# Kernel tuning notes

Hardware: AMD Instinct MI355X
Metric: run time of the kernel (lower is better)

The kernel has to match this reference:

```python
import jax, jax.numpy as jnp
import numpy as np

B, S, D, H = 2, 2048, 1024, 16
HD = D // H  # head_dim = 64


def setup_inputs() -> dict:
    key = jax.random.key(0)
    k1, k2, k3 = jax.random.split(key, 3)
    x = jax.random.normal(k1, (B, S, D), dtype=jnp.float32)
    mask = jnp.zeros((B, S, S), dtype=jnp.float32)  # additive mask
    # Dense(3*D) params (glorot-ish scale) and Dense(D) output projection
    Wqkv = jax.random.normal(k2, (D, 3 * D), dtype=jnp.float32) * (1.0 / np.sqrt(D))
    bqkv = jnp.zeros((3 * D,), dtype=jnp.float32)
    Wo = jax.random.normal(k3, (D, D), dtype=jnp.float32) * (1.0 / np.sqrt(D))
    bo = jnp.zeros((D,), dtype=jnp.float32)
    return {"x": x, "mask": mask, "Wqkv": Wqkv, "bqkv": bqkv, "Wo": Wo, "bo": bo}


def reference(x, mask, Wqkv, bqkv, Wo, bo):
    b, s, d = x.shape
    qkv = x @ Wqkv + bqkv                              # [B,S,3D]
    qkv = qkv.reshape(b, s, H, 3 * HD).transpose(0, 2, 1, 3)  # [B,H,S,3*HD]
    q, k, v = jnp.split(qkv, 3, axis=-1)               # each [B,H,S,HD]
    scale = 1.0 / jnp.sqrt(jnp.float32(HD))
    scores = jnp.einsum('bhqd,bhkd->bhqk', q, k) * scale  # [B,H,S,S]
    scores = scores + mask[:, None, :, :]
    attn = jax.nn.softmax(scores, axis=-1)
    values = jnp.einsum('bhqk,bhkd->bhqd', attn, v)    # [B,H,S,HD]
    # Faithful to original: reshape WITHOUT transposing heads back
    values = values.reshape(b, s, H * HD)              # [B,S,D]
    return values @ Wo + bo
```

## Files before the change

kernel.cpp:

```cpp
#include <hip/hip_runtime.h>
#include <hip/hip_bf16.h>

#define B_ 2
#define S_ 2048
#define D_ 1024
#define H_ 16
#define HD_ 64

typedef __attribute__((ext_vector_type(8))) short short8;
typedef __attribute__((ext_vector_type(4))) float f32x4;
typedef __attribute__((ext_vector_type(16))) float f32x16;
typedef __attribute__((ext_vector_type(4))) unsigned short us4;

static __device__ __forceinline__ ushort f2bf(float x) {
  __hip_bfloat16 h = __float2bfloat16(x);
  return *reinterpret_cast<ushort*>(&h);
}

static __device__ __forceinline__ void gld_lds16(void* lds, const void* g) {
  __builtin_amdgcn_global_load_lds(
      (__attribute__((address_space(1))) void*)(g),
      (__attribute__((address_space(3))) void*)(lds), 16, 0, 0);
}


__global__ __launch_bounds__(256) void cvt_bf16_vec(const float4* __restrict__ in,
                                                    ushort* __restrict__ out, int n4) {
  int i = blockIdx.x * blockDim.x + threadIdx.x;
  if (i < n4) {
    float4 v = in[i];
    ushort4 o;
    o.x = f2bf(v.x); o.y = f2bf(v.y); o.z = f2bf(v.z); o.w = f2bf(v.w);
    *reinterpret_cast<ushort4*>(out + (size_t)i * 4) = o;
  }
}

__global__ __launch_bounds__(256) void transpose_cvt(const float* __restrict__ in,
                                                     ushort* __restrict__ out,
                                                     int K, int N) {
  __shared__ float tile[32][33];
  const int bn = blockIdx.x * 32, bk = blockIdx.y * 32;
  const int tx = threadIdx.x, ty = threadIdx.y;
  #pragma unroll
  for (int i = ty; i < 32; i += 8)
    tile[i][tx] = in[(size_t)(bk + i) * N + bn + tx];
  __syncthreads();
  #pragma unroll
  for (int i = ty; i < 32; i += 8)
    out[(size_t)(bn + i) * K + bk + tx] = f2bf(tile[tx][i]);
}

template <bool OUT_BF16>
__global__ __launch_bounds__(256) void gemm_bt(const ushort* __restrict__ A,
                                               const ushort* __restrict__ Bt,
                                               const float* __restrict__ bias,
                                               ushort* __restrict__ Cb,
                                               float* __restrict__ Cf,
                                               int M, int N, int K) {
  __shared__ __align__(16) ushort As[128 * 32];
  __shared__ __align__(16) ushort Bs[128 * 32];
  const int tid = threadIdx.x;
  const int lane = tid & 63, wid = tid >> 6;
  const int wr = wid >> 1, wc = wid & 1;
  const int row0 = blockIdx.x * 128, col0 = blockIdx.y * 128;
  const int l15 = lane & 15, lhi = lane >> 4;

  f32x4 acc[4][4];
  #pragma unroll
  for (int i = 0; i < 4; ++i)
    #pragma unroll
    for (int j = 0; j < 4; ++j)
      acc[i][j] = f32x4{0.f, 0.f, 0.f, 0.f};

  const int sr = tid >> 2;
  const int scol = (tid & 3) * 8;

  for (int k0 = 0; k0 < K; k0 += 32) {
    gld_lds16(&As[(size_t)tid * 8],        &A[(size_t)(row0 + sr) * K + k0 + scol]);
    gld_lds16(&As[2048 + (size_t)tid * 8], &A[(size_t)(row0 + 64 + sr) * K + k0 + scol]);
    gld_lds16(&Bs[(size_t)tid * 8],        &Bt[(size_t)(col0 + sr) * K + k0 + scol]);
    gld_lds16(&Bs[2048 + (size_t)tid * 8], &Bt[(size_t)(col0 + 64 + sr) * K + k0 + scol]);
    __syncthreads();

    short8 af[4], bfr[4];
    #pragma unroll
    for (int mt = 0; mt < 4; ++mt)
      af[mt] = *(const short8*)&As[(wr * 64 + mt * 16 + l15) * 32 + lhi * 8];
    #pragma unroll
    for (int nt = 0; nt < 4; ++nt)
      bfr[nt] = *(const short8*)&Bs[(wc * 64 + nt * 16 + l15) * 32 + lhi * 8];
    #pragma unroll
    for (int mt = 0; mt < 4; ++mt)
      #pragma unroll
      for (int nt = 0; nt < 4; ++nt)
        acc[mt][nt] = __builtin_amdgcn_mfma_f32_16x16x32_bf16(af[mt], bfr[nt], acc[mt][nt], 0, 0, 0);
    __syncthreads();
  }

  const int orow = row0 + wr * 64;
  const int ocol = col0 + wc * 64 + l15;
  #pragma unroll
  for (int mt = 0; mt < 4; ++mt) {
    #pragma unroll
    for (int nt = 0; nt < 4; ++nt) {
      const int gc = ocol + nt * 16;
      const float bv = bias[gc];
      #pragma unroll
      for (int r = 0; r < 4; ++r) {
        const int gr = orow + mt * 16 + lhi * 4 + r;
        const float v = acc[mt][nt][r] + bv;
        if (OUT_BF16) Cb[(size_t)gr * N + gc] = f2bf(v);
        else          Cf[(size_t)gr * N + gc] = v;
      }
    }
  }
}

__global__ __launch_bounds__(256, 2) void flash_attn(const ushort* __restrict__ qkv,
                                                     const float* __restrict__ mask,
                                                     ushort* __restrict__ values) {
  __shared__ __align__(16) ushort Ks[2][64 * 64];
  __shared__ __align__(16) ushort Vt[2][64 * 64];

  const int tid = threadIdx.x;
  const int lane = tid & 63, wid = tid >> 6;
  const int l31 = lane & 31, lhalf = lane >> 5;
  const int qt = blockIdx.x, bh = blockIdx.y, b = bh >> 4, h = bh & 15;
  const size_t base = (size_t)b * S_ * 3072 + (size_t)h * 192;
  const int q = qt * 128 + wid * 32 + l31;

  short8 qf[4];
  {
    const ushort* qrow = qkv + base + (size_t)q * 3072 + lhalf * 8;
    qf[0] = *(const short8*)(qrow);
    qf[1] = *(const short8*)(qrow + 16);
    qf[2] = *(const short8*)(qrow + 32);
    qf[3] = *(const short8*)(qrow + 48);
  }

  const int srow = tid >> 3, sch = tid & 7;
  const int hsr = (srow ^ (srow >> 3)) & 7;
  const int scs = sch ^ hsr;
  const int kg = tid & 15, d0 = (tid >> 4) * 4;
  const int skg = (kg & 12) | ((kg & 1) << 1) | ((kg >> 1) & 1);

  float m_run = -3.0e38f, l_run = 0.f;
  f32x16 o[2];
  #pragma unroll
  for (int dg = 0; dg < 2; ++dg)
    #pragma unroll
    for (int i = 0; i < 16; ++i) o[dg][i] = 0.f;

  const float* mrow = mask + ((size_t)b * S_ + q) * S_;
  f32x4 mk[8], mkn[8];
  const int NT = S_ / 64;
  int cur = 0;
  us4 vr[4];

  {
    const ushort* kgp = qkv + base + (size_t)srow * 3072 + 64;
    gld_lds16(&Ks[0][tid * 8],        kgp + scs * 8);
    gld_lds16(&Ks[0][2048 + tid * 8], kgp + (size_t)32 * 3072 + (scs ^ 4) * 8);
    #pragma unroll
    for (int kk = 0; kk < 4; ++kk)
      vr[kk] = *(const us4*)(qkv + base + (size_t)(kg * 4 + kk) * 3072 + 128 + d0);
    #pragma unroll
    for (int i = 0; i < 8; ++i)
      mk[i] = *(const f32x4*)(mrow + (i >> 2) * 32 + (i & 3) * 8 + lhalf * 4);
    #pragma unroll
    for (int dd = 0; dd < 4; ++dd) {
      const int d = d0 + dd;
      const int hd = (d ^ (d >> 3)) & 7;
      us4 w;
      w[0] = vr[0][dd]; w[1] = vr[1][dd]; w[2] = vr[2][dd]; w[3] = vr[3][dd];
      *(us4*)&Vt[0][d * 64 + (((skg >> 1) ^ hd) & 7) * 8 + (skg & 1) * 4] = w;
    }
    __syncthreads();
  }

  for (int kt = 0; kt < NT; ++kt) {
    const int nxt = cur ^ 1;
    const bool pre = (kt + 1 < NT);

    if (pre) {
      const size_t nb = base + (size_t)(kt + 1) * 64 * 3072;
      const ushort* kgp = qkv + nb + (size_t)srow * 3072 + 64;
      gld_lds16(&Ks[nxt][tid * 8],        kgp + scs * 8);
      gld_lds16(&Ks[nxt][2048 + tid * 8], kgp + (size_t)32 * 3072 + (scs ^ 4) * 8);
      #pragma unroll
      for (int kk = 0; kk < 4; ++kk)
        vr[kk] = *(const us4*)(qkv + nb + (size_t)(kg * 4 + kk) * 3072 + 128 + d0);
      const float* mn = mrow + (size_t)(kt + 1) * 64;
      #pragma unroll
      for (int i = 0; i < 8; ++i)
        mkn[i] = *(const f32x4*)(mn + (i >> 2) * 32 + (i & 3) * 8 + lhalf * 4);
    }

    f32x16 sc[2];
    __builtin_amdgcn_s_setprio(1);
    #pragma unroll
    for (int g = 0; g < 2; ++g) {
      const int row = g * 32 + l31;
      const int hk = (row ^ (row >> 3)) & 7;
      const ushort* kp = &Ks[cur][row * 64];
      f32x16 s;
      #pragma unroll
      for (int i = 0; i < 16; ++i) s[i] = 0.f;
      #pragma unroll
      for (int kd = 0; kd < 4; ++kd) {
        short8 kf = *(const short8*)&kp[(((kd * 2 + lhalf) ^ hk) & 7) * 8];
        s = __builtin_amdgcn_mfma_f32_32x32x16_bf16(kf, qf[kd], s, 0, 0, 0);
      }
      sc[g] = s;
    }
    __builtin_amdgcn_s_setprio(0);

    #pragma unroll
    for (int g = 0; g < 2; ++g)
      #pragma unroll
      for (int r = 0; r < 16; ++r)
        sc[g][r] = sc[g][r] * 0.125f + mk[g * 4 + (r >> 2)][r & 3];

    float mx = sc[0][0];
    #pragma unroll
    for (int g = 0; g < 2; ++g)
      #pragma unroll
      for (int r = 0; r < 16; ++r) mx = fmaxf(mx, sc[g][r]);
    mx = fmaxf(mx, __shfl_xor(mx, 32));
    const float mnew = fmaxf(m_run, mx);
    const float alpha = __expf(m_run - mnew);
    m_run = mnew;
    float ps = 0.f;
    #pragma unroll
    for (int g = 0; g < 2; ++g)
      #pragma unroll
      for (int r = 0; r < 16; ++r) {
        const float p = __expf(sc[g][r] - mnew);
        sc[g][r] = p;
        ps += p;
      }
    ps += __shfl_xor(ps, 32);
    l_run = l_run * alpha + ps;
    #pragma unroll
    for (int dg = 0; dg < 2; ++dg)
      #pragma unroll
      for (int i = 0; i < 16; ++i) o[dg][i] *= alpha;

    short8 pf[4];
    #pragma unroll
    for (int ks = 0; ks < 4; ++ks)
      #pragma unroll
      for (int j = 0; j < 8; ++j)
        pf[ks][j] = (short)f2bf(sc[ks >> 1][8 * (ks & 1) + j]);

    __builtin_amdgcn_s_setprio(1);
    #pragma unroll
    for (int dg = 0; dg < 2; ++dg) {
      const int d = dg * 32 + l31;
      const int hv = (d ^ (d >> 3)) & 7;
      const ushort* vp = &Vt[cur][d * 64];
      #pragma unroll
      for (int ks = 0; ks < 4; ++ks) {
        short8 vf = *(const short8*)&vp[(((ks * 2 + lhalf) ^ hv) & 7) * 8];
        o[dg] = __builtin_amdgcn_mfma_f32_32x32x16_bf16(vf, pf[ks], o[dg], 0, 0, 0);
      }
    }
    __builtin_amdgcn_s_setprio(0);

    if (pre) {
      #pragma unroll
      for (int dd = 0; dd < 4; ++dd) {
        const int d = d0 + dd;
        const int hd = (d ^ (d >> 3)) & 7;
        us4 w;
        w[0] = vr[0][dd]; w[1] = vr[1][dd]; w[2] = vr[2][dd]; w[3] = vr[3][dd];
        *(us4*)&Vt[nxt][d * 64 + (((skg >> 1) ^ hd) & 7) * 8 + (skg & 1) * 4] = w;
      }
      #pragma unroll
      for (int i = 0; i < 8; ++i) mk[i] = mkn[i];
    }
    __syncthreads();
    cur = nxt;
  }

  const float inv = 1.0f / l_run;
  ushort* vout = values + ((size_t)bh * S_ + q) * 64;
  #pragma unroll
  for (int dg = 0; dg < 2; ++dg)
    #pragma unroll
    for (int quad = 0; quad < 4; ++quad) {
      us4 w;
      #pragma unroll
      for (int r = 0; r < 4; ++r) w[r] = f2bf(o[dg][quad * 4 + r] * inv);
      *(us4*)(vout + dg * 32 + quad * 8 + lhalf * 4) = w;
    }
}


extern "C" void kernel_launch(void* const* d_in, const int* in_sizes, int n_in,
                              void* d_out, int out_size, void* d_ws, size_t ws_size,
                              hipStream_t stream) {
  const float* x    = (const float*)d_in[0];
  const float* mask = (const float*)d_in[1];
  const float* Wqkv = (const float*)d_in[2];
  const float* bqkv = (const float*)d_in[3];
  const float* Wo   = (const float*)d_in[4];
  const float* bo   = (const float*)d_in[5];
  float* out = (float*)d_out;

  char* ws = (char*)d_ws;
  ushort* xbf    = (ushort*)(ws + 0);
  ushort* vals   = (ushort*)(ws + 0);
  ushort* wqkvT  = (ushort*)(ws + 8388608);
  ushort* woT    = (ushort*)(ws + 14680064);
  ushort* qkv    = (ushort*)(ws + 16777216);

  cvt_bf16_vec<<<4096, 256, 0, stream>>>((const float4*)x, xbf, (B_ * S_ * D_) / 4);
  transpose_cvt<<<dim3(3 * D_ / 32, D_ / 32), dim3(32, 8), 0, stream>>>(Wqkv, wqkvT, D_, 3 * D_);
  transpose_cvt<<<dim3(D_ / 32, D_ / 32), dim3(32, 8), 0, stream>>>(Wo, woT, D_, D_);
  gemm_bt<true><<<dim3((B_ * S_) / 128, (3 * D_) / 128), 256, 0, stream>>>(
      xbf, wqkvT, bqkv, qkv, nullptr, B_ * S_, 3 * D_, D_);
  flash_attn<<<dim3(S_ / 128, B_ * H_), 256, 0, stream>>>(qkv, mask, vals);
  gemm_bt<false><<<dim3((B_ * S_) / 128, D_ / 128), 256, 0, stream>>>(
      vals, woT, bo, nullptr, out, B_ * S_, D_, D_);
}
```

Measured before the change: 180.4 us.

## Process 128-key tiles per iteration with lazy softmax rescaling in flash attention

Doubles the key/value tile per loop iteration from 64 to 128 keys, with double-buffered LDS holding two 64-key subtiles per stage. This halves the number of barriers and softmax reductions per key. It also switches to a conditional online-softmax rescale that only updates the running max when it grows by more than 8, skipping the exponential and the accumulator multiply in most iterations. The mask is now loaded at the start of each iteration instead of being prefetched one tile ahead. This increases register pressure (16 mask vectors, 4 score tiles, 8 V staging registers) and LDS use to 64KB per block, which may lower occupancy under launch_bounds(256,2).

```diff
diff --git a/kernel.cpp b/kernel.cpp
--- a/kernel.cpp
+++ b/kernel.cpp
@@ -119,8 +119,8 @@
 __global__ __launch_bounds__(256, 2) void flash_attn(const ushort* __restrict__ qkv,
                                                      const float* __restrict__ mask,
                                                      ushort* __restrict__ values) {
-  __shared__ __align__(16) ushort Ks[2][64 * 64];
-  __shared__ __align__(16) ushort Vt[2][64 * 64];
+  __shared__ __align__(16) ushort Ks[2][2][64 * 64];
+  __shared__ __align__(16) ushort Vt[2][2][64 * 64];
 
   const int tid = threadIdx.x;
   const int lane = tid & 63, wid = tid >> 6;
@@ -152,132 +152,152 @@
     for (int i = 0; i < 16; ++i) o[dg][i] = 0.f;
 
   const float* mrow = mask + ((size_t)b * S_ + q) * S_;
-  f32x4 mk[8], mkn[8];
-  const int NT = S_ / 64;
+  const int NT2 = S_ / 128;
   int cur = 0;
-  us4 vr[4];
+  us4 vr[8];
 
   {
-    const ushort* kgp = qkv + base + (size_t)srow * 3072 + 64;
-    gld_lds16(&Ks[0][tid * 8],        kgp + scs * 8);
-    gld_lds16(&Ks[0][2048 + tid * 8], kgp + (size_t)32 * 3072 + (scs ^ 4) * 8);
-    #pragma unroll
-    for (int kk = 0; kk < 4; ++kk)
-      vr[kk] = *(const us4*)(qkv + base + (size_t)(kg * 4 + kk) * 3072 + 128 + d0);
-    #pragma unroll
-    for (int i = 0; i < 8; ++i)
-      mk[i] = *(const f32x4*)(mrow + (i >> 2) * 32 + (i & 3) * 8 + lhalf * 4);
-    #pragma unroll
-    for (int dd = 0; dd < 4; ++dd) {
-      const int d = d0 + dd;
-      const int hd = (d ^ (d >> 3)) & 7;
-      us4 w;
-      w[0] = vr[0][dd]; w[1] = vr[1][dd]; w[2] = vr[2][dd]; w[3] = vr[3][dd];
-      *(us4*)&Vt[0][d * 64 + (((skg >> 1) ^ hd) & 7) * 8 + (skg & 1) * 4] = w;
-    }
-    __syncthreads();
-  }
-
-  for (int kt = 0; kt < NT; ++kt) {
-    const int nxt = cur ^ 1;
-    const bool pre = (kt + 1 < NT);
-
-    if (pre) {
-      const size_t nb = base + (size_t)(kt + 1) * 64 * 3072;
-      const ushort* kgp = qkv + nb + (size_t)srow * 3072 + 64;
-      gld_lds16(&Ks[nxt][tid * 8],        kgp + scs * 8);
-      gld_lds16(&Ks[nxt][2048 + tid * 8], kgp + (size_t)32 * 3072 + (scs ^ 4) * 8);
+    #pragma unroll
+    for (int s2 = 0; s2 < 2; ++s2) {
+      const ushort* kgp = qkv + base + (size_t)(s2 * 64 + srow) * 3072 + 64;
+      gld_lds16(&Ks[0][s2][tid * 8],        kgp + scs * 8);
+      gld_lds16(&Ks[0][s2][2048 + tid * 8], kgp + (size_t)32 * 3072 + (scs ^ 4) * 8);
       #pragma unroll
       for (int kk = 0; kk < 4; ++kk)
-        vr[kk] = *(const us4*)(qkv + nb + (size_t)(kg * 4 + kk) * 3072 + 128 + d0);
-      const float* mn = mrow + (size_t)(kt + 1) * 64;
-      #pragma unroll
-      for (int i = 0; i < 8; ++i)
-        mkn[i] = *(const f32x4*)(mn + (i >> 2) * 32 + (i & 3) * 8 + lhalf * 4);
-    }
-
-    f32x16 sc[2];
-    __builtin_amdgcn_s_setprio(1);
-    #pragma unroll
-    for (int g = 0; g < 2; ++g) {
-      const int row = g * 32 + l31;
-      const int hk = (row ^ (row >> 3)) & 7;
-      const ushort* kp = &Ks[cur][row * 64];
-      f32x16 s;
-      #pragma unroll
-      for (int i = 0; i < 16; ++i) s[i] = 0.f;
-      #pragma unroll
-      for (int kd = 0; kd < 4; ++kd) {
-        short8 kf = *(const short8*)&kp[(((kd * 2 + lhalf) ^ hk) & 7) * 8];
-        s = __builtin_amdgcn_mfma_f32_32x32x16_bf16(kf, qf[kd], s, 0, 0, 0);
-      }
-      sc[g] = s;
-    }
-    __builtin_amdgcn_s_setprio(0);
-
-    #pragma unroll
-    for (int g = 0; g < 2; ++g)
-      #pragma unroll
-      for (int r = 0; r < 16; ++r)
-        sc[g][r] = sc[g][r] * 0.125f + mk[g * 4 + (r >> 2)][r & 3];
-
-    float mx = sc[0][0];
-    #pragma unroll
-    for (int g = 0; g < 2; ++g)
-      #pragma unroll
-      for (int r = 0; r < 16; ++r) mx = fmaxf(mx, sc[g][r]);
-    mx = fmaxf(mx, __shfl_xor(mx, 32));
-    const float mnew = fmaxf(m_run, mx);
-    const float alpha = __expf(m_run - mnew);
-    m_run = mnew;
-    float ps = 0.f;
-    #pragma unroll
-    for (int g = 0; g < 2; ++g)
-      #pragma unroll
-      for (int r = 0; r < 16; ++r) {
-        const float p = __expf(sc[g][r] - mnew);
-        sc[g][r] = p;
-        ps += p;
-      }
-    ps += __shfl_xor(ps, 32);
-    l_run = l_run * alpha + ps;
-    #pragma unroll
-    for (int dg = 0; dg < 2; ++dg)
-      #pragma unroll
-      for (int i = 0; i < 16; ++i) o[dg][i] *= alpha;
-
-    short8 pf[4];
-    #pragma unroll
-    for (int ks = 0; ks < 4; ++ks)
-      #pragma unroll
-      for (int j = 0; j < 8; ++j)
-        pf[ks][j] = (short)f2bf(sc[ks >> 1][8 * (ks & 1) + j]);
-
-    __builtin_amdgcn_s_setprio(1);
-    #pragma unroll
-    for (int dg = 0; dg < 2; ++dg) {
-      const int d = dg * 32 + l31;
-      const int hv = (d ^ (d >> 3)) & 7;
-      const ushort* vp = &Vt[cur][d * 64];
-      #pragma unroll
-      for (int ks = 0; ks < 4; ++ks) {
-        short8 vf = *(const short8*)&vp[(((ks * 2 + lhalf) ^ hv) & 7) * 8];
-        o[dg] = __builtin_amdgcn_mfma_f32_32x32x16_bf16(vf, pf[ks], o[dg], 0, 0, 0);
-      }
-    }
-    __builtin_amdgcn_s_setprio(0);
-
-    if (pre) {
+        vr[s2 * 4 + kk] = *(const us4*)(qkv + base +
+                           (size_t)(s2 * 64 + kg * 4 + kk) * 3072 + 128 + d0);
+    }
+    #pragma unroll
+    for (int s2 = 0; s2 < 2; ++s2)
       #pragma unroll
       for (int dd = 0; dd < 4; ++dd) {
         const int d = d0 + dd;
         const int hd = (d ^ (d >> 3)) & 7;
         us4 w;
-        w[0] = vr[0][dd]; w[1] = vr[1][dd]; w[2] = vr[2][dd]; w[3] = vr[3][dd];
-        *(us4*)&Vt[nxt][d * 64 + (((skg >> 1) ^ hd) & 7) * 8 + (skg & 1) * 4] = w;
-      }
-      #pragma unroll
-      for (int i = 0; i < 8; ++i) mk[i] = mkn[i];
+        w[0] = vr[s2 * 4 + 0][dd]; w[1] = vr[s2 * 4 + 1][dd];
+        w[2] = vr[s2 * 4 + 2][dd]; w[3] = vr[s2 * 4 + 3][dd];
+        *(us4*)&Vt[0][s2][d * 64 + (((skg >> 1) ^ hd) & 7) * 8 + (skg & 1) * 4] = w;
+      }
+    __syncthreads();
+  }
+
+  for (int t = 0; t < NT2; ++t) {
+    const int nxt = cur ^ 1;
+    const bool pre = (t + 1 < NT2);
+
+    f32x4 mk[16];
+    {
+      const float* mp0 = mrow + (size_t)t * 128 + lhalf * 4;
+      #pragma unroll
+      for (int i = 0; i < 16; ++i)
+        mk[i] = *(const f32x4*)(mp0 + (i >> 3) * 64 + ((i >> 2) & 1) * 32 + (i & 3) * 8);
+    }
+
+    if (pre) {
+      const size_t nb = base + (size_t)(t + 1) * 128 * 3072;
+      #pragma unroll
+      for (int s2 = 0; s2 < 2; ++s2) {
+        const ushort* kgp = qkv + nb + (size_t)(s2 * 64 + srow) * 3072 + 64;
+        gld_lds16(&Ks[nxt][s2][tid * 8],        kgp + scs * 8);
+        gld_lds16(&Ks[nxt][s2][2048 + tid * 8], kgp + (size_t)32 * 3072 + (scs ^ 4) * 8);
+        #pragma unroll
+        for (int kk = 0; kk < 4; ++kk)
+          vr[s2 * 4 + kk] = *(const us4*)(qkv + nb +
+                             (size_t)(s2 * 64 + kg * 4 + kk) * 3072 + 128 + d0);
+      }
+    }
+
+    f32x16 sc[4];
+    __builtin_amdgcn_s_setprio(1);
+    #pragma unroll
+    for (int s2 = 0; s2 < 2; ++s2)
+      #pragma unroll
+      for (int g = 0; g < 2; ++g) {
+        const int row = g * 32 + l31;
+        const int hk = (row ^ (row >> 3)) & 7;
+        const ushort* kp = &Ks[cur][s2][row * 64];
+        f32x16 s;
+        #pragma unroll
+        for (int i = 0; i < 16; ++i) s[i] = 0.f;
+        #pragma unroll
+        for (int kd = 0; kd < 4; ++kd) {
+          short8 kf = *(const short8*)&kp[(((kd * 2 + lhalf) ^ hk) & 7) * 8];
+          s = __builtin_amdgcn_mfma_f32_32x32x16_bf16(kf, qf[kd], s, 0, 0, 0);
+        }
+        sc[s2 * 2 + g] = s;
+      }
+    __builtin_amdgcn_s_setprio(0);
+
+    #pragma unroll
+    for (int c4 = 0; c4 < 4; ++c4)
+      #pragma unroll
+      for (int r = 0; r < 16; ++r)
+        sc[c4][r] = sc[c4][r] * 0.125f + mk[(c4 >> 1) * 8 + (c4 & 1) * 4 + (r >> 2)][r & 3];
+
+    float mx = sc[0][0];
+    #pragma unroll
+    for (int c4 = 0; c4 < 4; ++c4)
+      #pragma unroll
+      for (int r = 0; r < 16; ++r) mx = fmaxf(mx, sc[c4][r]);
+    mx = fmaxf(mx, __shfl_xor(mx, 32));
+    if (__any(mx > m_run + 8.0f)) {
+      const float mnew = fmaxf(m_run, mx);
+      const float alpha = __expf(m_run - mnew);
+      m_run = mnew;
+      l_run *= alpha;
+      #pragma unroll
+      for (int dg = 0; dg < 2; ++dg)
+        #pragma unroll
+        for (int i = 0; i < 16; ++i) o[dg][i] *= alpha;
+    }
+    float ps = 0.f;
+    #pragma unroll
+    for (int c4 = 0; c4 < 4; ++c4)
+      #pragma unroll
+      for (int r = 0; r < 16; ++r) {
+        const float p = __expf(sc[c4][r] - m_run);
+        sc[c4][r] = p;
+        ps += p;
+      }
+    ps += __shfl_xor(ps, 32);
+    l_run += ps;
+
+    short8 pf[8];
+    #pragma unroll
+    for (int ks = 0; ks < 8; ++ks) {
+      const int sub = ks >> 2, k2 = ks & 3;
+      #pragma unroll
+      for (int j = 0; j < 8; ++j)
+        pf[ks][j] = (short)f2bf(sc[sub * 2 + (k2 >> 1)][8 * (k2 & 1) + j]);
+    }
+
+    __builtin_amdgcn_s_setprio(1);
+    #pragma unroll
+    for (int dg = 0; dg < 2; ++dg) {
+      const int d = dg * 32 + l31;
+      const int hv = (d ^ (d >> 3)) & 7;
+      #pragma unroll
+      for (int ks = 0; ks < 8; ++ks) {
+        const int sub = ks >> 2, kl = ks & 3;
+        const ushort* vp = &Vt[cur][sub][d * 64];
+        short8 vf = *(const short8*)&vp[(((kl * 2 + lhalf) ^ hv) & 7) * 8];
+        o[dg] = __builtin_amdgcn_mfma_f32_32x32x16_bf16(vf, pf[ks], o[dg], 0, 0, 0);
+      }
+    }
+    __builtin_amdgcn_s_setprio(0);
+
+    if (pre) {
+      #pragma unroll
+      for (int s2 = 0; s2 < 2; ++s2)
+        #pragma unroll
+        for (int dd = 0; dd < 4; ++dd) {
+          const int d = d0 + dd;
+          const int hd = (d ^ (d >> 3)) & 7;
+          us4 w;
+          w[0] = vr[s2 * 4 + 0][dd]; w[1] = vr[s2 * 4 + 1][dd];
+          w[2] = vr[s2 * 4 + 2][dd]; w[3] = vr[s2 * 4 + 3][dd];
+          *(us4*)&Vt[nxt][s2][d * 64 + (((skg >> 1) ^ hd) & 7) * 8 + (skg & 1) * 4] = w;
+        }
     }
     __syncthreads();
     cur = nxt;
```

New measurement: 196.7 us. +9.0%, slower.

## Split attention over key halves with combine kernel and lazy rescaling

Applied to the files above, without the earlier changes.

Adds a split-KV flash attention variant that runs each query tile over half of the keys, doubling the grid, and writes fp32 partial outputs plus running max and sum. A separate combine kernel merges the two halves into bf16 values. The split path is used only when the workspace is large enough. It also skips the output rescale unless the running max grows by more than a threshold, and loads the mask per tile instead of double-buffering it in registers. The goal is more blocks in flight and fewer rescale multiplies, at the cost of extra fp32 global traffic and one more kernel launch.

```diff
diff --git a/kernel.cpp b/kernel.cpp
--- a/kernel.cpp
+++ b/kernel.cpp
@@ -116,16 +116,18 @@
   }
 }
 
-__global__ __launch_bounds__(256, 2) void flash_attn(const ushort* __restrict__ qkv,
-                                                     const float* __restrict__ mask,
-                                                     ushort* __restrict__ values) {
+__global__ __launch_bounds__(256, 4) void flash_attn_split(const ushort* __restrict__ qkv,
+                                                           const float* __restrict__ mask,
+                                                           float* __restrict__ po,
+                                                           float2* __restrict__ ml) {
   __shared__ __align__(16) ushort Ks[2][64 * 64];
   __shared__ __align__(16) ushort Vt[2][64 * 64];
 
   const int tid = threadIdx.x;
   const int lane = tid & 63, wid = tid >> 6;
   const int l31 = lane & 31, lhalf = lane >> 5;
-  const int qt = blockIdx.x, bh = blockIdx.y, b = bh >> 4, h = bh & 15;
+  const int qt = blockIdx.x, bh = blockIdx.y, half = blockIdx.z;
+  const int b = bh >> 4, h = bh & 15;
   const size_t base = (size_t)b * S_ * 3072 + (size_t)h * 192;
   const int q = qt * 128 + wid * 32 + l31;
 
@@ -151,22 +153,22 @@
     #pragma unroll
     for (int i = 0; i < 16; ++i) o[dg][i] = 0.f;
 
-  const float* mrow = mask + ((size_t)b * S_ + q) * S_;
-  f32x4 mk[8], mkn[8];
-  const int NT = S_ / 64;
+  const float* mrow = mask + ((size_t)b * S_ + q) * S_ + half * 1024;
+  const int NT = 16;
   int cur = 0;
   us4 vr[4];
 
+  const ushort* kstage = qkv + base + (size_t)half * 1024 * 3072 + (size_t)srow * 3072 + 64;
+  const ushort* vload  = qkv + base + (size_t)half * 1024 * 3072 + (size_t)(kg * 4) * 3072 + 128 + d0;
+
   {
-    const ushort* kgp = qkv + base + (size_t)srow * 3072 + 64;
-    gld_lds16(&Ks[0][tid * 8],        kgp + scs * 8);
-    gld_lds16(&Ks[0][2048 + tid * 8], kgp + (size_t)32 * 3072 + (scs ^ 4) * 8);
+    gld_lds16(&Ks[0][tid * 8],        kstage + scs * 8);
+    gld_lds16(&Ks[0][2048 + tid * 8], kstage + (size_t)32 * 3072 + (scs ^ 4) * 8);
     #pragma unroll
     for (int kk = 0; kk < 4; ++kk)
-      vr[kk] = *(const us4*)(qkv + base + (size_t)(kg * 4 + kk) * 3072 + 128 + d0);
-    #pragma unroll
-    for (int i = 0; i < 8; ++i)
-      mk[i] = *(const f32x4*)(mrow + (i >> 2) * 32 + (i & 3) * 8 + lhalf * 4);
+      vr[kk] = *(const us4*)(vload + (size_t)kk * 3072);
+    kstage += (size_t)64 * 3072;
+    vload  += (size_t)64 * 3072;
     #pragma unroll
     for (int dd = 0; dd < 4; ++dd) {
       const int d = d0 + dd;
@@ -183,17 +185,21 @@
     const bool pre = (kt + 1 < NT);
 
     if (pre) {
-      const size_t nb = base + (size_t)(kt + 1) * 64 * 3072;
-      const ushort* kgp = qkv + nb + (size_t)srow * 3072 + 64;
-      gld_lds16(&Ks[nxt][tid * 8],        kgp + scs * 8);
-      gld_lds16(&Ks[nxt][2048 + tid * 8], kgp + (size_t)32 * 3072 + (scs ^ 4) * 8);
+      gld_lds16(&Ks[nxt][tid * 8],        kstage + scs * 8);
+      gld_lds16(&Ks[nxt][2048 + tid * 8], kstage + (size_t)32 * 3072 + (scs ^ 4) * 8);
       #pragma unroll
       for (int kk = 0; kk < 4; ++kk)
-        vr[kk] = *(const us4*)(qkv + nb + (size_t)(kg * 4 + kk) * 3072 + 128 + d0);
-      const float* mn = mrow + (size_t)(kt + 1) * 64;
+        vr[kk] = *(const us4*)(vload + (size_t)kk * 3072);
+      kstage += (size_t)64 * 3072;
+      vload  += (size_t)64 * 3072;
+    }
+
+    f32x4 mk[8];
+    {
+      const float* mp = mrow + kt * 64 + lhalf * 4;
       #pragma unroll
       for (int i = 0; i < 8; ++i)
-        mkn[i] = *(const f32x4*)(mn + (i >> 2) * 32 + (i & 3) * 8 + lhalf * 4);
+        mk[i] = *(const f32x4*)(mp + (i >> 2) * 32 + (i & 3) * 8);
     }
 
     f32x16 sc[2];
@@ -227,24 +233,27 @@
       #pragma unroll
       for (int r = 0; r < 16; ++r) mx = fmaxf(mx, sc[g][r]);
     mx = fmaxf(mx, __shfl_xor(mx, 32));
-    const float mnew = fmaxf(m_run, mx);
-    const float alpha = __expf(m_run - mnew);
-    m_run = mnew;
+    if (__any(mx > m_run + 8.0f)) {
+      const float mnew = fmaxf(m_run, mx);
+      const float alpha = __expf(m_run - mnew);
+      m_run = mnew;
+      l_run *= alpha;
+      #pragma unroll
+      for (int dg = 0; dg < 2; ++dg)
+        #pragma unroll
+        for (int i = 0; i < 16; ++i) o[dg][i] *= alpha;
+    }
     float ps = 0.f;
     #pragma unroll
     for (int g = 0; g < 2; ++g)
       #pragma unroll
       for (int r = 0; r < 16; ++r) {
-        const float p = __expf(sc[g][r] - mnew);
+        const float p = __expf(sc[g][r] - m_run);
         sc[g][r] = p;
         ps += p;
       }
     ps += __shfl_xor(ps, 32);
-    l_run = l_run * alpha + ps;
-    #pragma unroll
-    for (int dg = 0; dg < 2; ++dg)
-      #pragma unroll
-      for (int i = 0; i < 16; ++i) o[dg][i] *= alpha;
+    l_run += ps;
 
     short8 pf[4];
     #pragma unroll
@@ -276,8 +285,206 @@
         w[0] = vr[0][dd]; w[1] = vr[1][dd]; w[2] = vr[2][dd]; w[3] = vr[3][dd];
         *(us4*)&Vt[nxt][d * 64 + (((skg >> 1) ^ hd) & 7) * 8 + (skg & 1) * 4] = w;
       }
-      #pragma unroll
-      for (int i = 0; i < 8; ++i) mk[i] = mkn[i];
+    }
+    __syncthreads();
+    cur = nxt;
+  }
+
+  const size_t prow_i = (size_t)half * 65536 + (size_t)bh * S_ + q;
+  float* prow = po + prow_i * 64;
+  #pragma unroll
+  for (int dg = 0; dg < 2; ++dg)
+    #pragma unroll
+    for (int quad = 0; quad < 4; ++quad) {
+      f32x4 w;
+      #pragma unroll
+      for (int r = 0; r < 4; ++r) w[r] = o[dg][quad * 4 + r];
+      *(f32x4*)(prow + dg * 32 + quad * 8 + lhalf * 4) = w;
+    }
+  if (lhalf == 0) ml[prow_i] = make_float2(m_run, l_run);
+}
+
+__global__ __launch_bounds__(256) void combine_halves(const float* __restrict__ po,
+                                                      const float2* __restrict__ ml,
+                                                      ushort* __restrict__ vals) {
+  const int idx = blockIdx.x * 256 + threadIdx.x;
+  const int qr = idx >> 4, c = idx & 15;
+  const float2 a = ml[qr];
+  const float2 bml = ml[65536 + qr];
+  const float m = fmaxf(a.x, bml.x);
+  const float w0 = __expf(a.x - m), w1 = __expf(bml.x - m);
+  const float inv = 1.0f / (a.y * w0 + bml.y * w1);
+  const f32x4 o0 = *(const f32x4*)(po + (size_t)qr * 64 + c * 4);
+  const f32x4 o1 = *(const f32x4*)(po + (size_t)(65536 + qr) * 64 + c * 4);
+  us4 w;
+  #pragma unroll
+  for (int r = 0; r < 4; ++r) w[r] = f2bf((o0[r] * w0 + o1[r] * w1) * inv);
+  *(us4*)(vals + (size_t)qr * 64 + c * 4) = w;
+}
+
+__global__ __launch_bounds__(256, 2) void flash_attn(const ushort* __restrict__ qkv,
+                                                     const float* __restrict__ mask,
+                                                     ushort* __restrict__ values) {
+  __shared__ __align__(16) ushort Ks[2][64 * 64];
+  __shared__ __align__(16) ushort Vt[2][64 * 64];
+
+  const int tid = threadIdx.x;
+  const int lane = tid & 63, wid = tid >> 6;
+  const int l31 = lane & 31, lhalf = lane >> 5;
+  const int qt = blockIdx.x, bh = blockIdx.y, b = bh >> 4, h = bh & 15;
+  const size_t base = (size_t)b * S_ * 3072 + (size_t)h * 192;
+  const int q = qt * 128 + wid * 32 + l31;
+
+  short8 qf[4];
+  {
+    const ushort* qrow = qkv + base + (size_t)q * 3072 + lhalf * 8;
+    qf[0] = *(const short8*)(qrow);
+    qf[1] = *(const short8*)(qrow + 16);
+    qf[2] = *(const short8*)(qrow + 32);
+    qf[3] = *(const short8*)(qrow + 48);
+  }
+
+  const int srow = tid >> 3, sch = tid & 7;
+  const int hsr = (srow ^ (srow >> 3)) & 7;
+  const int scs = sch ^ hsr;
+  const int kg = tid & 15, d0 = (tid >> 4) * 4;
+  const int skg = (kg & 12) | ((kg & 1) << 1) | ((kg >> 1) & 1);
+
+  float m_run = -3.0e38f, l_run = 0.f;
+  f32x16 o[2];
+  #pragma unroll
+  for (int dg = 0; dg < 2; ++dg)
+    #pragma unroll
+    for (int i = 0; i < 16; ++i) o[dg][i] = 0.f;
+
+  const float* mrow = mask + ((size_t)b * S_ + q) * S_;
+  const int NT = S_ / 64;
+  int cur = 0;
+  us4 vr[4];
+
+  {
+    const ushort* kgp = qkv + base + (size_t)srow * 3072 + 64;
+    gld_lds16(&Ks[0][tid * 8],        kgp + scs * 8);
+    gld_lds16(&Ks[0][2048 + tid * 8], kgp + (size_t)32 * 3072 + (scs ^ 4) * 8);
+    #pragma unroll
+    for (int kk = 0; kk < 4; ++kk)
+      vr[kk] = *(const us4*)(qkv + base + (size_t)(kg * 4 + kk) * 3072 + 128 + d0);
+    #pragma unroll
+    for (int dd = 0; dd < 4; ++dd) {
+      const int d = d0 + dd;
+      const int hd = (d ^ (d >> 3)) & 7;
+      us4 w;
+      w[0] = vr[0][dd]; w[1] = vr[1][dd]; w[2] = vr[2][dd]; w[3] = vr[3][dd];
+      *(us4*)&Vt[0][d * 64 + (((skg >> 1) ^ hd) & 7) * 8 + (skg & 1) * 4] = w;
+    }
+    __syncthreads();
+  }
+
+  for (int kt = 0; kt < NT; ++kt) {
+    const int nxt = cur ^ 1;
+    const bool pre = (kt + 1 < NT);
+
+    if (pre) {
+      const size_t nb = base + (size_t)(kt + 1) * 64 * 3072;
+      const ushort* kgp = qkv + nb + (size_t)srow * 3072 + 64;
+      gld_lds16(&Ks[nxt][tid * 8],        kgp + scs * 8);
+      gld_lds16(&Ks[nxt][2048 + tid * 8], kgp + (size_t)32 * 3072 + (scs ^ 4) * 8);
+      #pragma unroll
+      for (int kk = 0; kk < 4; ++kk)
+        vr[kk] = *(const us4*)(qkv + nb + (size_t)(kg * 4 + kk) * 3072 + 128 + d0);
+    }
+
+    f32x4 mk[8];
+    {
+      const float* mp = mrow + kt * 64 + lhalf * 4;
+      #pragma unroll
+      for (int i = 0; i < 8; ++i)
+        mk[i] = *(const f32x4*)(mp + (i >> 2) * 32 + (i & 3) * 8);
+    }
+
+    f32x16 sc[2];
+    __builtin_amdgcn_s_setprio(1);
+    #pragma unroll
+    for (int g = 0; g < 2; ++g) {
+      const int row = g * 32 + l31;
+      const int hk = (row ^ (row >> 3)) & 7;
+      const ushort* kp = &Ks[cur][row * 64];
+      f32x16 s;
+      #pragma unroll
+      for (int i = 0; i < 16; ++i) s[i] = 0.f;
+      #pragma unroll
+      for (int kd = 0; kd < 4; ++kd) {
+        short8 kf = *(const short8*)&kp[(((kd * 2 + lhalf) ^ hk) & 7) * 8];
+        s = __builtin_amdgcn_mfma_f32_32x32x16_bf16(kf, qf[kd], s, 0, 0, 0);
+      }
+      sc[g] = s;
+    }
+    __builtin_amdgcn_s_setprio(0);
+
+    #pragma unroll
+    for (int g = 0; g < 2; ++g)
+      #pragma unroll
+      for (int r = 0; r < 16; ++r)
+        sc[g][r] = sc[g][r] * 0.125f + mk[g * 4 + (r >> 2)][r & 3];
+
+    float mx = sc[0][0];
+    #pragma unroll
+    for (int g = 0; g < 2; ++g)
+      #pragma unroll
+      for (int r = 0; r < 16; ++r) mx = fmaxf(mx, sc[g][r]);
+    mx = fmaxf(mx, __shfl_xor(mx, 32));
+    if (__any(mx > m_run + 8.0f)) {
+      const float mnew = fmaxf(m_run, mx);
+      const float alpha = __expf(m_run - mnew);
+      m_run = mnew;
+      l_run *= alpha;
+      #pragma unroll
+      for (int dg = 0; dg < 2; ++dg)
+        #pragma unroll
+        for (int i = 0; i < 16; ++i) o[dg][i] *= alpha;
+    }
+    float ps = 0.f;
+    #pragma unroll
+    for (int g = 0; g < 2; ++g)
+      #pragma unroll
+      for (int r = 0; r < 16; ++r) {
+        const float p = __expf(sc[g][r] - m_run);
+        sc[g][r] = p;
+        ps += p;
+      }
+    ps += __shfl_xor(ps, 32);
+    l_run += ps;
+
+    short8 pf[4];
+    #pragma unroll
+    for (int ks = 0; ks < 4; ++ks)
+      #pragma unroll
+      for (int j = 0; j < 8; ++j)
+        pf[ks][j] = (short)f2bf(sc[ks >> 1][8 * (ks & 1) + j]);
+
+    __builtin_amdgcn_s_setprio(1);
+    #pragma unroll
+    for (int dg = 0; dg < 2; ++dg) {
+      const int d = dg * 32 + l31;
+      const int hv = (d ^ (d >> 3)) & 7;
+      const ushort* vp = &Vt[cur][d * 64];
+      #pragma unroll
+      for (int ks = 0; ks < 4; ++ks) {
+        short8 vf = *(const short8*)&vp[(((ks * 2 + lhalf) ^ hv) & 7) * 8];
+        o[dg] = __builtin_amdgcn_mfma_f32_32x32x16_bf16(vf, pf[ks], o[dg], 0, 0, 0);
+      }
+    }
+    __builtin_amdgcn_s_setprio(0);
+
+    if (pre) {
+      #pragma unroll
+      for (int dd = 0; dd < 4; ++dd) {
+        const int d = d0 + dd;
+        const int hd = (d ^ (d >> 3)) & 7;
+        us4 w;
+        w[0] = vr[0][dd]; w[1] = vr[1][dd]; w[2] = vr[2][dd]; w[3] = vr[3][dd];
+        *(us4*)&Vt[nxt][d * 64 + (((skg >> 1) ^ hd) & 7) * 8 + (skg & 1) * 4] = w;
+      }
     }
     __syncthreads();
     cur = nxt;
@@ -314,13 +521,21 @@
   ushort* wqkvT  = (ushort*)(ws + 8388608);
   ushort* woT    = (ushort*)(ws + 14680064);
   ushort* qkv    = (ushort*)(ws + 16777216);
+  float*  po     = (float*)(ws + 41943040);
+  float2* ml     = (float2*)(ws + 75497472);
+  const bool split_ok = (ws_size >= 76546048ull);
 
   cvt_bf16_vec<<<4096, 256, 0, stream>>>((const float4*)x, xbf, (B_ * S_ * D_) / 4);
   transpose_cvt<<<dim3(3 * D_ / 32, D_ / 32), dim3(32, 8), 0, stream>>>(Wqkv, wqkvT, D_, 3 * D_);
   transpose_cvt<<<dim3(D_ / 32, D_ / 32), dim3(32, 8), 0, stream>>>(Wo, woT, D_, D_);
   gemm_bt<true><<<dim3((B_ * S_) / 128, (3 * D_) / 128), 256, 0, stream>>>(
       xbf, wqkvT, bqkv, qkv, nullptr, B_ * S_, 3 * D_, D_);
-  flash_attn<<<dim3(S_ / 128, B_ * H_), 256, 0, stream>>>(qkv, mask, vals);
+  if (split_ok) {
+    flash_attn_split<<<dim3(S_ / 128, B_ * H_, 2), 256, 0, stream>>>(qkv, mask, po, ml);
+    combine_halves<<<4096, 256, 0, stream>>>(po, ml, vals);
+  } else {
+    flash_attn<<<dim3(S_ / 128, B_ * H_), 256, 0, stream>>>(qkv, mask, vals);
+  }
   gemm_bt<false><<<dim3((B_ * S_) / 128, D_ / 128), 256, 0, stream>>>(
       vals, woT, bo, nullptr, out, B_ * S_, D_, D_);
 }
```

Result: slower. 261.1 us (+44.7%).

## Software-pipeline QK^T one tile ahead and skip rescale with lazy max threshold

Applied to the files above, without the earlier changes.

Restructures the flash-attention loop so the QK^T MFMAs for tile t+1 are issued alongside the softmax and PV of tile t, with K prefetched two tiles ahead and the loop unrolled by two to ping-pong score registers. The aim is to hide the exp/max vector work behind matrix-core work. The online-softmax rescale of the output accumulators is now done only when the new max exceeds the running max by more than 8, which skips most alpha multiplies. The mask load moves to the current iteration instead of being double-buffered in registers. Together these raise register pressure and could spill or reduce occupancy.

```diff
diff --git a/kernel.cpp b/kernel.cpp
--- a/kernel.cpp
+++ b/kernel.cpp
@@ -128,6 +128,7 @@
   const int qt = blockIdx.x, bh = blockIdx.y, b = bh >> 4, h = bh & 15;
   const size_t base = (size_t)b * S_ * 3072 + (size_t)h * 192;
   const int q = qt * 128 + wid * 32 + l31;
+  const int NT = S_ / 64;
 
   short8 qf[4];
   {
@@ -152,135 +153,139 @@
     for (int i = 0; i < 16; ++i) o[dg][i] = 0.f;
 
   const float* mrow = mask + ((size_t)b * S_ + q) * S_;
-  f32x4 mk[8], mkn[8];
-  const int NT = S_ / 64;
-  int cur = 0;
   us4 vr[4];
+  f32x16 scA[2], scB[2];
+
+#define QKT_(SCDST, KSBUF)                                                     \
+  {                                                                            \
+    _Pragma("unroll")                                                          \
+    for (int g = 0; g < 2; ++g) {                                              \
+      const int row_ = g * 32 + l31;                                           \
+      const int hk_ = (row_ ^ (row_ >> 3)) & 7;                                \
+      const ushort* kp_ = &(KSBUF)[row_ * 64];                                 \
+      f32x16 s_;                                                               \
+      _Pragma("unroll")                                                        \
+      for (int i = 0; i < 16; ++i) s_[i] = 0.f;                                \
+      _Pragma("unroll")                                                        \
+      for (int kd = 0; kd < 4; ++kd) {                                         \
+        short8 kf_ = *(const short8*)&kp_[(((kd * 2 + lhalf) ^ hk_) & 7) * 8]; \
+        s_ = __builtin_amdgcn_mfma_f32_32x32x16_bf16(kf_, qf[kd], s_, 0, 0, 0);\
+      }                                                                        \
+      (SCDST)[g] = s_;                                                         \
+    }                                                                          \
+  }
+
+#define VSCATTER_(VTBUF)                                                       \
+  {                                                                            \
+    _Pragma("unroll")                                                          \
+    for (int dd = 0; dd < 4; ++dd) {                                           \
+      const int d_ = d0 + dd;                                                  \
+      const int hd_ = (d_ ^ (d_ >> 3)) & 7;                                    \
+      us4 w_;                                                                  \
+      w_[0] = vr[0][dd]; w_[1] = vr[1][dd];                                    \
+      w_[2] = vr[2][dd]; w_[3] = vr[3][dd];                                    \
+      *(us4*)&(VTBUF)[d_ * 64 + (((skg >> 1) ^ hd_) & 7) * 8 + (skg & 1) * 4] = w_; \
+    }                                                                          \
+  }
+
+#define HALF_(T, SCCUR, SCNEXT)                                                \
+  {                                                                            \
+    const int t_ = (T);                                                        \
+    const bool pre1_ = (t_ + 1 < NT), pre2_ = (t_ + 2 < NT);                   \
+    if (pre2_) {                                                               \
+      const ushort* kn_ = qkv + base + (size_t)(t_ + 2) * 64 * 3072 +          \
+                          (size_t)srow * 3072 + 64;                            \
+      gld_lds16(&Ks[t_ & 1][tid * 8],        kn_ + scs * 8);                   \
+      gld_lds16(&Ks[t_ & 1][2048 + tid * 8], kn_ + (size_t)32 * 3072 + (scs ^ 4) * 8); \
+    }                                                                          \
+    if (pre1_) {                                                               \
+      const ushort* vn_ = qkv + base + (size_t)(t_ + 1) * 64 * 3072 + 128 + d0;\
+      _Pragma("unroll")                                                        \
+      for (int kk = 0; kk < 4; ++kk)                                           \
+        vr[kk] = *(const us4*)(vn_ + (size_t)(kg * 4 + kk) * 3072);            \
+    }                                                                          \
+    f32x4 mk_[8];                                                              \
+    {                                                                          \
+      const float* mp_ = mrow + t_ * 64 + lhalf * 4;                           \
+      _Pragma("unroll")                                                        \
+      for (int i = 0; i < 8; ++i)                                              \
+        mk_[i] = *(const f32x4*)(mp_ + (i >> 2) * 32 + (i & 3) * 8);           \
+    }                                                                          \
+    __builtin_amdgcn_s_setprio(1);                                             \
+    if (pre1_) QKT_(SCNEXT, Ks[(t_ + 1) & 1]);                                 \
+                     \
+    _Pragma("unroll")                                                          \
+    for (int g = 0; g < 2; ++g)                                                \
+      _Pragma("unroll")                                                        \
+      for (int r = 0; r < 16; ++r)                                             \
+        (SCCUR)[g][r] = (SCCUR)[g][r] * 0.125f + mk_[g * 4 + (r >> 2)][r & 3]; \
+    float mx_ = (SCCUR)[0][0];                                                 \
+    _Pragma("unroll")                                                          \
+    for (int g = 0; g < 2; ++g)                                                \
+      _Pragma("unroll")                                                        \
+      for (int r = 0; r < 16; ++r) mx_ = fmaxf(mx_, (SCCUR)[g][r]);            \
+    mx_ = fmaxf(mx_, __shfl_xor(mx_, 32));                                     \
+    if (__any(mx_ > m_run + 8.0f)) {                                           \
+      const float mnew_ = fmaxf(m_run, mx_);                                   \
+      const float alpha_ = __expf(m_run - mnew_);                              \
+      m_run = mnew_;                                                           \
+      l_run *= alpha_;                                                         \
+      _Pragma("unroll")                                                        \
+      for (int dg = 0; dg < 2; ++dg)                                           \
+        _Pragma("unroll")                                                      \
+        for (int i = 0; i < 16; ++i) o[dg][i] *= alpha_;                       \
+    }                                                                          \
+    float ps_ = 0.f;                                                           \
+    _Pragma("unroll")                                                          \
+    for (int g = 0; g < 2; ++g)                                                \
+      _Pragma("unroll")                                                        \
+      for (int r = 0; r < 16; ++r) {                                           \
+        const float p_ = __expf((SCCUR)[g][r] - m_run);                        \
+        (SCCUR)[g][r] = p_;                                                    \
+        ps_ += p_;                                                             \
+      }                                                                        \
+    ps_ += __shfl_xor(ps_, 32);                                                \
+    l_run += ps_;                                                              \
+    short8 pf_[4];                                                             \
+    _Pragma("unroll")                                                          \
+    for (int ks = 0; ks < 4; ++ks)                                             \
+      _Pragma("unroll")                                                        \
+      for (int j = 0; j < 8; ++j)                                              \
+        pf_[ks][j] = (short)f2bf((SCCUR)[ks >> 1][8 * (ks & 1) + j]);          \
+    _Pragma("unroll")                                                          \
+    for (int dg = 0; dg < 2; ++dg) {                                           \
+      const int d_ = dg * 32 + l31;                                            \
+      const int hv_ = (d_ ^ (d_ >> 3)) & 7;                                    \
+      const ushort* vp_ = &Vt[t_ & 1][d_ * 64];                                \
+      _Pragma("unroll")                                                        \
+      for (int ks = 0; ks < 4; ++ks) {                                         \
+        short8 vf_ = *(const short8*)&vp_[(((ks * 2 + lhalf) ^ hv_) & 7) * 8]; \
+        o[dg] = __builtin_amdgcn_mfma_f32_32x32x16_bf16(vf_, pf_[ks], o[dg], 0, 0, 0); \
+      }                                                                        \
+    }                                                                          \
+    __builtin_amdgcn_s_setprio(0);                                             \
+    if (pre1_) VSCATTER_(Vt[(t_ + 1) & 1]);                                    \
+    __syncthreads();                                                           \
+  }
 
   {
-    const ushort* kgp = qkv + base + (size_t)srow * 3072 + 64;
-    gld_lds16(&Ks[0][tid * 8],        kgp + scs * 8);
-    gld_lds16(&Ks[0][2048 + tid * 8], kgp + (size_t)32 * 3072 + (scs ^ 4) * 8);
+    const ushort* k0 = qkv + base + (size_t)srow * 3072 + 64;
+    gld_lds16(&Ks[0][tid * 8],        k0 + scs * 8);
+    gld_lds16(&Ks[0][2048 + tid * 8], k0 + (size_t)32 * 3072 + (scs ^ 4) * 8);
+    const ushort* k1 = k0 + (size_t)64 * 3072;
+    gld_lds16(&Ks[1][tid * 8],        k1 + scs * 8);
+    gld_lds16(&Ks[1][2048 + tid * 8], k1 + (size_t)32 * 3072 + (scs ^ 4) * 8);
     #pragma unroll
     for (int kk = 0; kk < 4; ++kk)
       vr[kk] = *(const us4*)(qkv + base + (size_t)(kg * 4 + kk) * 3072 + 128 + d0);
-    #pragma unroll
-    for (int i = 0; i < 8; ++i)
-      mk[i] = *(const f32x4*)(mrow + (i >> 2) * 32 + (i & 3) * 8 + lhalf * 4);
-    #pragma unroll
-    for (int dd = 0; dd < 4; ++dd) {
-      const int d = d0 + dd;
-      const int hd = (d ^ (d >> 3)) & 7;
-      us4 w;
-      w[0] = vr[0][dd]; w[1] = vr[1][dd]; w[2] = vr[2][dd]; w[3] = vr[3][dd];
-      *(us4*)&Vt[0][d * 64 + (((skg >> 1) ^ hd) & 7) * 8 + (skg & 1) * 4] = w;
-    }
+    VSCATTER_(Vt[0]);
     __syncthreads();
-  }
-
-  for (int kt = 0; kt < NT; ++kt) {
-    const int nxt = cur ^ 1;
-    const bool pre = (kt + 1 < NT);
-
-    if (pre) {
-      const size_t nb = base + (size_t)(kt + 1) * 64 * 3072;
-      const ushort* kgp = qkv + nb + (size_t)srow * 3072 + 64;
-      gld_lds16(&Ks[nxt][tid * 8],        kgp + scs * 8);
-      gld_lds16(&Ks[nxt][2048 + tid * 8], kgp + (size_t)32 * 3072 + (scs ^ 4) * 8);
-      #pragma unroll
-      for (int kk = 0; kk < 4; ++kk)
-        vr[kk] = *(const us4*)(qkv + nb + (size_t)(kg * 4 + kk) * 3072 + 128 + d0);
-      const float* mn = mrow + (size_t)(kt + 1) * 64;
-      #pragma unroll
-      for (int i = 0; i < 8; ++i)
-        mkn[i] = *(const f32x4*)(mn + (i >> 2) * 32 + (i & 3) * 8 + lhalf * 4);
-    }
-
-    f32x16 sc[2];
-    __builtin_amdgcn_s_setprio(1);
-    #pragma unroll
-    for (int g = 0; g < 2; ++g) {
-      const int row = g * 32 + l31;
-      const int hk = (row ^ (row >> 3)) & 7;
-      const ushort* kp = &Ks[cur][row * 64];
-      f32x16 s;
-      #pragma unroll
-      for (int i = 0; i < 16; ++i) s[i] = 0.f;
-      #pragma unroll
-      for (int kd = 0; kd < 4; ++kd) {
-        short8 kf = *(const short8*)&kp[(((kd * 2 + lhalf) ^ hk) & 7) * 8];
-        s = __builtin_amdgcn_mfma_f32_32x32x16_bf16(kf, qf[kd], s, 0, 0, 0);
-      }
-      sc[g] = s;
-    }
-    __builtin_amdgcn_s_setprio(0);
-
-    #pragma unroll
-    for (int g = 0; g < 2; ++g)
-      #pragma unroll
-      for (int r = 0; r < 16; ++r)
-        sc[g][r] = sc[g][r] * 0.125f + mk[g * 4 + (r >> 2)][r & 3];
-
-    float mx = sc[0][0];
-    #pragma unroll
-    for (int g = 0; g < 2; ++g)
-      #pragma unroll
-      for (int r = 0; r < 16; ++r) mx = fmaxf(mx, sc[g][r]);
-    mx = fmaxf(mx, __shfl_xor(mx, 32));
-    const float mnew = fmaxf(m_run, mx);
-    const float alpha = __expf(m_run - mnew);
-    m_run = mnew;
-    float ps = 0.f;
-    #pragma unroll
-    for (int g = 0; g < 2; ++g)
-      #pragma unroll
-      for (int r = 0; r < 16; ++r) {
-        const float p = __expf(sc[g][r] - mnew);
-        sc[g][r] = p;
-        ps += p;
-      }
-    ps += __shfl_xor(ps, 32);
-    l_run = l_run * alpha + ps;
-    #pragma unroll
-    for (int dg = 0; dg < 2; ++dg)
-      #pragma unroll
-      for (int i = 0; i < 16; ++i) o[dg][i] *= alpha;
-
-    short8 pf[4];
-    #pragma unroll
-    for (int ks = 0; ks < 4; ++ks)
-      #pragma unroll
-      for (int j = 0; j < 8; ++j)
-        pf[ks][j] = (short)f2bf(sc[ks >> 1][8 * (ks & 1) + j]);
-
-    __builtin_amdgcn_s_setprio(1);
-    #pragma unroll
-    for (int dg = 0; dg < 2; ++dg) {
-      const int d = dg * 32 + l31;
-      const int hv = (d ^ (d >> 3)) & 7;
-      const ushort* vp = &Vt[cur][d * 64];
-      #pragma unroll
-      for (int ks = 0; ks < 4; ++ks) {
-        short8 vf = *(const short8*)&vp[(((ks * 2 + lhalf) ^ hv) & 7) * 8];
-        o[dg] = __builtin_amdgcn_mfma_f32_32x32x16_bf16(vf, pf[ks], o[dg], 0, 0, 0);
-      }
-    }
-    __builtin_amdgcn_s_setprio(0);
-
-    if (pre) {
-      #pragma unroll
-      for (int dd = 0; dd < 4; ++dd) {
-        const int d = d0 + dd;
-        const int hd = (d ^ (d >> 3)) & 7;
-        us4 w;
-        w[0] = vr[0][dd]; w[1] = vr[1][dd]; w[2] = vr[2][dd]; w[3] = vr[3][dd];
-        *(us4*)&Vt[nxt][d * 64 + (((skg >> 1) ^ hd) & 7) * 8 + (skg & 1) * 4] = w;
-      }
-      #pragma unroll
-      for (int i = 0; i < 8; ++i) mk[i] = mkn[i];
-    }
-    __syncthreads();
-    cur = nxt;
+    QKT_(scA, Ks[0]);
+  }
+
+  for (int tp = 0; tp < NT; tp += 2) {
+    HALF_(tp,     scA, scB);
+    HALF_(tp + 1, scB, scA);
   }
 
   const float inv = 1.0f / l_run;
@@ -294,6 +299,9 @@
       for (int r = 0; r < 4; ++r) w[r] = f2bf(o[dg][quad * 4 + r] * inv);
       *(us4*)(vout + dg * 32 + quad * 8 + lhalf * 4) = w;
     }
+#undef HALF_
+#undef VSCATTER_
+#undef QKT_
 }
 
 
```

After: 184.4 us. 1.02x slower.
